# Performance work log

Hardware: AMD Instinct MI355X
Metric: run time of the kernel (lower is better)

## Reference

```python
import jax, jax.numpy as jnp
import numpy as np

B, T, D, H = 4, 2048, 1024, 16
HD = D // H  # head_dim = 64


def setup_inputs() -> dict:
    key = jax.random.key(0)
    k1, k2, k3 = jax.random.split(key, 3)
    x = jax.random.normal(k1, (B, T, D), dtype=jnp.float32)
    # Linear weights stored [in, out] (transpose of torch's [out, in]); scaled init.
    w_qkv = jax.random.normal(k2, (D, 3 * D), dtype=jnp.float32) / np.sqrt(D)
    b_qkv = jnp.zeros((3 * D,), dtype=jnp.float32)
    w_out = jax.random.normal(k3, (D, D), dtype=jnp.float32) / np.sqrt(D)
    b_out = jnp.zeros((D,), dtype=jnp.float32)
    # Causal mask [1,1,T,T]: 1 where attention allowed (j<=i), 0 elsewhere.
    causal_mask = jnp.tril(jnp.ones((T, T), dtype=jnp.int32))[None, None]
    return {"x": x, "causal_mask": causal_mask, "w_qkv": w_qkv,
            "b_qkv": b_qkv, "w_out": w_out, "b_out": b_out}


def reference(x, causal_mask, w_qkv, b_qkv, w_out, b_out):
    b, t, c = x.shape
    qkv = x @ w_qkv + b_qkv                         # [B,T,3D]
    qkv = qkv.reshape(b, t, 3, H, HD)
    q, k, v = jnp.moveaxis(qkv, 2, 0)               # each [B,T,H,HD]
    q = q.transpose(0, 2, 1, 3)                     # [B,H,T,HD]
    k = k.transpose(0, 2, 1, 3)
    v = v.transpose(0, 2, 1, 3)
    att = jnp.einsum('bhqd,bhkd->bhqk', q, k) / np.sqrt(HD).astype(np.float32)
    att = jnp.where(causal_mask == 0, jnp.float32(-jnp.inf), att)
    att = jax.nn.softmax(att, axis=-1)              # dropout=0.0 (eval)
    y = jnp.einsum('bhqk,bhkd->bhqd', att, v)       # [B,H,T,HD]
    y = y.transpose(0, 2, 1, 3).reshape(b, t, c)    # [B,T,D]
    return y @ w_out + b_out
```

## Files before the change

kernel.cpp:

```cpp
#include <hip/hip_runtime.h>
#include <hip/hip_bf16.h>
#include <stdint.h>

#define BB 4
#define TT 2048
#define DD 1024
#define HH 16
#define HDD 64
#define M1 (BB*TT)
#define N1 (3*DD)
#define KDIM DD

typedef __attribute__((ext_vector_type(8))) short short8;
typedef __attribute__((ext_vector_type(4))) float f32x4;

#if __has_builtin(__builtin_amdgcn_exp2f)
#define EXP2(x) __builtin_amdgcn_exp2f(x)
#else
#define EXP2(x) exp2f(x)
#endif

#define GLOAD_LDS16(gp, lp) \
    __builtin_amdgcn_global_load_lds( \
        (const __attribute__((address_space(1))) void*)(gp), \
        (__attribute__((address_space(3))) void*)(lp), 16, 0, 0)

__device__ __forceinline__ float bf2f(unsigned short u) {
    union { uint32_t u32; float f; } c; c.u32 = ((uint32_t)u) << 16; return c.f;
}
__device__ __forceinline__ unsigned short f2bf(float f) {
    union { float f; uint32_t u32; } c; c.f = f;
    uint32_t u = c.u32;
    return (unsigned short)((u + 0x7FFFu + ((u >> 16) & 1u)) >> 16);
}

template <int CTRL>
__device__ __forceinline__ float dpp_ror(float x) {
    union { float f; int i; } u, r;
    u.f = x;
    r.i = __builtin_amdgcn_update_dpp(u.i, u.i, CTRL, 0xF, 0xF, false);
    return r.f;
}
__device__ __forceinline__ float red_max16(float x) {
    x = fmaxf(x, dpp_ror<0x128>(x));
    x = fmaxf(x, dpp_ror<0x124>(x));
    x = fmaxf(x, dpp_ror<0x122>(x));
    x = fmaxf(x, dpp_ror<0x121>(x));
    return x;
}
__device__ __forceinline__ float red_sum16(float x) {
    x += dpp_ror<0x128>(x);
    x += dpp_ror<0x124>(x);
    x += dpp_ror<0x122>(x);
    x += dpp_ror<0x121>(x);
    return x;
}

__global__ __launch_bounds__(256) void cvt_f32_bf16(
    const float* __restrict__ in, unsigned short* __restrict__ out, int n4)
{
    int i = blockIdx.x * 256 + threadIdx.x;
    if (i >= n4) return;
    float4 v = *(const float4*)&in[(size_t)i * 4];
    ushort4 o;
    o.x = f2bf(v.x); o.y = f2bf(v.y); o.z = f2bf(v.z); o.w = f2bf(v.w);
    *(ushort4*)&out[(size_t)i * 4] = o;
}

__global__ __launch_bounds__(256) void transpose_f32_bf16(
    const float* __restrict__ in, unsigned short* __restrict__ out,
    int R, int C)
{
    __shared__ unsigned short tile[32][33];
    int bx = blockIdx.x;
    int by = blockIdx.y;
    int x = bx*32 + threadIdx.x;
    int y0 = by*32 + threadIdx.y;
    #pragma unroll
    for (int i = 0; i < 32; i += 8)
        tile[threadIdx.y + i][threadIdx.x] = f2bf(in[(size_t)(y0 + i)*C + x]);
    __syncthreads();
    int xo = by*32 + threadIdx.x;
    int yo = bx*32 + threadIdx.y;
    #pragma unroll
    for (int i = 0; i < 32; i += 8)
        out[(size_t)(yo + i)*R + xo] = tile[threadIdx.x][threadIdx.y + i];
}

#define GTSTR 264
template <int MODE>
__global__ __launch_bounds__(512, 2) void gemm8p(
    const unsigned short* __restrict__ A, const unsigned short* __restrict__ BT,
    const float* __restrict__ bias, void* __restrict__ Cout, void* __restrict__ Cout2,
    int K, int N, int NXT)
{
    constexpr int SHSZ = (MODE == 2) ? 256*GTSTR : 65536;
    __shared__ __align__(16) unsigned short Sh[SHSZ];

    const int tid  = threadIdx.x;
    const int lane = tid & 63;
    const int wave = tid >> 6;
    const int wm = wave >> 2, wn = wave & 3;
    const int quad = lane >> 4, l16 = lane & 15;

    const int nwg = gridDim.x, cpx = nwg >> 3;
    const int wg = (blockIdx.x & 7)*cpx + (blockIdx.x >> 3);
    const int by = wg / NXT, bx = wg - by*NXT;
    const int m0 = by*256, n0 = bx*256;

    f32x4 acc[8][4] = {};
    const int nk = K >> 6;

    auto SA = [&](int d, int h) -> unsigned short* { return &Sh[(d*2 + h)*16384]; };
    auto SB = [&](int d, int h) -> unsigned short* { return &Sh[(d*2 + h)*16384 + 8192]; };

    auto STG_A = [&](int d, int h, int t) {
        const int k0 = t << 6;
        unsigned short* dst = SA(d, h);
        #pragma unroll
        for (int p = 0; p < 2; ++p) {
            int c = p*512 + tid;
            int rl = c >> 3, ch = (c & 7) ^ (rl & 7);
            GLOAD_LDS16(&A[(size_t)(m0 + h*128 + rl)*K + k0 + ch*8], &dst[c*8]);
        }
    };
    auto STG_B = [&](int d, int h, int t) {
        const int k0 = t << 6;
        unsigned short* dst = SB(d, h);
        #pragma unroll
        for (int p = 0; p < 2; ++p) {
            int c = p*512 + tid;
            int rl = c >> 3, ch = (c & 7) ^ (rl & 7);
            GLOAD_LDS16(&BT[(size_t)(n0 + h*128 + rl)*K + k0 + ch*8], &dst[c*8]);
        }
    };
    auto RA = [&](int d, int mf, int kk) -> short8 {
        int rl = mf*16 + l16;
        return *(const short8*)&SA(d, wm)[rl*64 + (((kk*4 + quad) ^ (rl & 7))*8)];
    };
    auto RB = [&](int d, int nf, int kk) -> short8 {
        int rl = (wn & 1)*64 + nf*16 + l16;
        return *(const short8*)&SB(d, wn >> 1)[rl*64 + (((kk*4 + quad) ^ (rl & 7))*8)];
    };

    STG_A(0, 0, 0); STG_A(0, 1, 0); STG_B(0, 0, 0); STG_B(0, 1, 0);
    STG_A(1, 0, 1);
    asm volatile("s_waitcnt vmcnt(2)" ::: "memory");
    __builtin_amdgcn_s_barrier();
    __builtin_amdgcn_sched_barrier(0);

    for (int i = 0; i < nk/2; ++i) {
        const int tb = 2*i + 1, tn0 = 2*i + 2, tn1 = 2*i + 3;
        const bool p2 = (tn0 < nk), p3 = (tn1 < nk);
        short8 a0[4][2], a1[4][2], b0[2][2], b1[2][2];

        #pragma unroll
        for (int mf = 0; mf < 4; ++mf) { a0[mf][0] = RA(0, mf, 0); a0[mf][1] = RA(0, mf, 1); }
        #pragma unroll
        for (int nf = 0; nf < 2; ++nf) { b0[nf][0] = RB(0, nf, 0); b0[nf][1] = RB(0, nf, 1); }
        STG_A(1, 1, tb);
        __builtin_amdgcn_s_barrier();
        __builtin_amdgcn_s_setprio(1);
        #pragma unroll
        for (int mf = 0; mf < 4; ++mf)
            #pragma unroll
            for (int nf = 0; nf < 2; ++nf)
                #pragma unroll
                for (int kk = 0; kk < 2; ++kk)
                    acc[mf][nf] = __builtin_amdgcn_mfma_f32_16x16x32_bf16(
                        a0[mf][kk], b0[nf][kk], acc[mf][nf], 0, 0, 0);
        __builtin_amdgcn_s_setprio(0);
        __builtin_amdgcn_s_barrier();

        #pragma unroll
        for (int nf = 0; nf < 2; ++nf) { b1[nf][0] = RB(0, 2+nf, 0); b1[nf][1] = RB(0, 2+nf, 1); }
        STG_B(1, 0, tb);
        __builtin_amdgcn_s_barrier();
        __builtin_amdgcn_s_setprio(1);
        #pragma unroll
        for (int mf = 0; mf < 4; ++mf)
            #pragma unroll
            for (int nf = 0; nf < 2; ++nf)
                #pragma unroll
                for (int kk = 0; kk < 2; ++kk)
                    acc[mf][2+nf] = __builtin_amdgcn_mfma_f32_16x16x32_bf16(
                        a0[mf][kk], b1[nf][kk], acc[mf][2+nf], 0, 0, 0);
        __builtin_amdgcn_s_setprio(0);
        __builtin_amdgcn_s_barrier();

        #pragma unroll
        for (int mf = 0; mf < 4; ++mf) { a1[mf][0] = RA(0, 4+mf, 0); a1[mf][1] = RA(0, 4+mf, 1); }
        STG_B(1, 1, tb);
        __builtin_amdgcn_s_barrier();
        __builtin_amdgcn_s_setprio(1);
        #pragma unroll
        for (int mf = 0; mf < 4; ++mf)
            #pragma unroll
            for (int nf = 0; nf < 2; ++nf)
                #pragma unroll
                for (int kk = 0; kk < 2; ++kk)
                    acc[4+mf][nf] = __builtin_amdgcn_mfma_f32_16x16x32_bf16(
                        a1[mf][kk], b0[nf][kk], acc[4+mf][nf], 0, 0, 0);
        __builtin_amdgcn_s_setprio(0);
        __builtin_amdgcn_s_barrier();

        if (p2) STG_A(0, 0, tn0);
        __builtin_amdgcn_s_barrier();
        __builtin_amdgcn_s_setprio(1);
        #pragma unroll
        for (int mf = 0; mf < 4; ++mf)
            #pragma unroll
            for (int nf = 0; nf < 2; ++nf)
                #pragma unroll
                for (int kk = 0; kk < 2; ++kk)
                    acc[4+mf][2+nf] = __builtin_amdgcn_mfma_f32_16x16x32_bf16(
                        a1[mf][kk], b1[nf][kk], acc[4+mf][2+nf], 0, 0, 0);
        __builtin_amdgcn_s_setprio(0);
        if (p2) asm volatile("s_waitcnt vmcnt(2)" ::: "memory");
        else    asm volatile("s_waitcnt vmcnt(0)" ::: "memory");
        __builtin_amdgcn_s_barrier();
        __builtin_amdgcn_sched_barrier(0);

        #pragma unroll
        for (int mf = 0; mf < 4; ++mf) { a0[mf][0] = RA(1, mf, 0); a0[mf][1] = RA(1, mf, 1); }
        #pragma unroll
        for (int nf = 0; nf < 2; ++nf) { b0[nf][0] = RB(1, nf, 0); b0[nf][1] = RB(1, nf, 1); }
        if (p2) STG_A(0, 1, tn0);
        __builtin_amdgcn_s_barrier();
        __builtin_amdgcn_s_setprio(1);
        #pragma unroll
        for (int mf = 0; mf < 4; ++mf)
            #pragma unroll
            for (int nf = 0; nf < 2; ++nf)
                #pragma unroll
                for (int kk = 0; kk < 2; ++kk)
                    acc[mf][nf] = __builtin_amdgcn_mfma_f32_16x16x32_bf16(
                        a0[mf][kk], b0[nf][kk], acc[mf][nf], 0, 0, 0);
        __builtin_amdgcn_s_setprio(0);
        __builtin_amdgcn_s_barrier();

        #pragma unroll
        for (int nf = 0; nf < 2; ++nf) { b1[nf][0] = RB(1, 2+nf, 0); b1[nf][1] = RB(1, 2+nf, 1); }
        if (p2) STG_B(0, 0, tn0);
        __builtin_amdgcn_s_barrier();
        __builtin_amdgcn_s_setprio(1);
        #pragma unroll
        for (int mf = 0; mf < 4; ++mf)
            #pragma unroll
            for (int nf = 0; nf < 2; ++nf)
                #pragma unroll
                for (int kk = 0; kk < 2; ++kk)
                    acc[mf][2+nf] = __builtin_amdgcn_mfma_f32_16x16x32_bf16(
                        a0[mf][kk], b1[nf][kk], acc[mf][2+nf], 0, 0, 0);
        __builtin_amdgcn_s_setprio(0);
        __builtin_amdgcn_s_barrier();

        #pragma unroll
        for (int mf = 0; mf < 4; ++mf) { a1[mf][0] = RA(1, 4+mf, 0); a1[mf][1] = RA(1, 4+mf, 1); }
        if (p2) STG_B(0, 1, tn0);
        __builtin_amdgcn_s_barrier();
        __builtin_amdgcn_s_setprio(1);
        #pragma unroll
        for (int mf = 0; mf < 4; ++mf)
            #pragma unroll
            for (int nf = 0; nf < 2; ++nf)
                #pragma unroll
                for (int kk = 0; kk < 2; ++kk)
                    acc[4+mf][nf] = __builtin_amdgcn_mfma_f32_16x16x32_bf16(
                        a1[mf][kk], b0[nf][kk], acc[4+mf][nf], 0, 0, 0);
        __builtin_amdgcn_s_setprio(0);
        __builtin_amdgcn_s_barrier();

        if (p3) STG_A(1, 0, tn1);
        __builtin_amdgcn_s_barrier();
        __builtin_amdgcn_s_setprio(1);
        #pragma unroll
        for (int mf = 0; mf < 4; ++mf)
            #pragma unroll
            for (int nf = 0; nf < 2; ++nf)
                #pragma unroll
                for (int kk = 0; kk < 2; ++kk)
                    acc[4+mf][2+nf] = __builtin_amdgcn_mfma_f32_16x16x32_bf16(
                        a1[mf][kk], b1[nf][kk], acc[4+mf][2+nf], 0, 0, 0);
        __builtin_amdgcn_s_setprio(0);
        if (p3) asm volatile("s_waitcnt vmcnt(2)" ::: "memory");
        else    asm volatile("s_waitcnt vmcnt(0)" ::: "memory");
        __builtin_amdgcn_s_barrier();
        __builtin_amdgcn_sched_barrier(0);
    }

    if (MODE == 2 && n0 >= 2048) {
        #pragma unroll
        for (int ni = 0; ni < 4; ++ni) {
            int nl = wn*64 + ni*16 + l16;
            float bv = bias[n0 + nl];
            #pragma unroll
            for (int mi = 0; mi < 8; ++mi) {
                ushort4 pk;
                pk.x = f2bf(acc[mi][ni][0] + bv);
                pk.y = f2bf(acc[mi][ni][1] + bv);
                pk.z = f2bf(acc[mi][ni][2] + bv);
                pk.w = f2bf(acc[mi][ni][3] + bv);
                *(ushort4*)&Sh[nl*GTSTR + wm*128 + mi*16 + quad*4] = pk;
            }
        }
        __builtin_amdgcn_s_barrier();
        const int bb = m0 >> 11, t0 = m0 & 2047;
        #pragma unroll
        for (int p = 0; p < 16; ++p) {
            int c = p*512 + tid;
            int row = c >> 5, ch = c & 31;
            int nv = n0 + row - 2048;
            int hv = nv >> 6, dv = nv & 63;
            *(uint4*)&((unsigned short*)Cout2)[((size_t)((bb*16 + hv)*64 + dv))*2048 + t0 + ch*8] =
                *(uint4*)&Sh[row*GTSTR + ch*8];
        }
        return;
    }

    const int cstride = (MODE == 2) ? 2048 : N;
    #pragma unroll
    for (int ni = 0; ni < 4; ++ni) {
        int n = n0 + wn*64 + ni*16 + l16;
        float bv = bias[n];
        #pragma unroll
        for (int mi = 0; mi < 8; ++mi) {
            #pragma unroll
            for (int r = 0; r < 4; ++r) {
                int m = m0 + wm*128 + mi*16 + quad*4 + r;
                float val = acc[mi][ni][r] + bv;
                if (MODE == 1)
                    ((float*)Cout)[(size_t)m*cstride + n] = val;
                else
                    ((unsigned short*)Cout)[(size_t)m*cstride + n] = f2bf(val);
            }
        }
    }
}

template <int MODE, int BM, int BN>
__global__ __launch_bounds__(512, 2) void gemm_big(
    const unsigned short* __restrict__ A, const unsigned short* __restrict__ BT,
    const float* __restrict__ bias, void* __restrict__ Cout, void* __restrict__ Cout2,
    int K, int N, int NXT)
{
    constexpr int SHSZ = 2*(BM+BN)*64;
    __shared__ __align__(16) unsigned short Sh[SHSZ];

    const int tid  = threadIdx.x;
    const int lane = tid & 63;
    const int wave = tid >> 6;
    constexpr int WNG = BN/64;
    const int wm = wave / WNG, wn = wave % WNG;
    const int quad = lane >> 4, l16 = lane & 15;

    const int nwg = gridDim.x, cpx = nwg >> 3;
    const int wg = (blockIdx.x & 7)*cpx + (blockIdx.x >> 3);
    const int by = wg / NXT, bx = wg - by*NXT;
    const int m0 = by*BM, n0 = bx*BN;

    f32x4 acc[4][4] = {};
    const int nk = K >> 6;

    auto STAGE = [&](int t, int buf) {
        const int k0 = t << 6;
        unsigned short* Ab = &Sh[buf*(BM*64)];
        unsigned short* Bb = &Sh[2*BM*64 + buf*(BN*64)];
        #pragma unroll
        for (int p = 0; p < BM/64; ++p) {
            int c = p*512 + tid;
            int row = c >> 3, ch = (c & 7) ^ (row & 7);
            GLOAD_LDS16(&A[(size_t)(m0 + row)*K + k0 + ch*8], &Ab[c*8]);
        }
        #pragma unroll
        for (int p = 0; p < BN/64; ++p) {
            int c = p*512 + tid;
            int row = c >> 3, ch = (c & 7) ^ (row & 7);
            GLOAD_LDS16(&BT[(size_t)(n0 + row)*K + k0 + ch*8], &Bb[c*8]);
        }
    };

    STAGE(0, 0);
    STAGE(1, 1);

    for (int t = 0; t < nk; ++t) {
        const int buf = t & 1;
        const unsigned short* Ab = &Sh[buf*(BM*64)];
        const unsigned short* Bb = &Sh[2*BM*64 + buf*(BN*64)];

        if (t == nk - 1) asm volatile("s_waitcnt vmcnt(0)" ::: "memory");
        else             asm volatile("s_waitcnt vmcnt(6)" ::: "memory");
        __builtin_amdgcn_s_barrier();
        __builtin_amdgcn_sched_barrier(0);

        short8 fa[4][2], fb[2][2];

        #pragma unroll
        for (int mi = 0; mi < 4; ++mi)
            #pragma unroll
            for (int kk = 0; kk < 2; ++kk) {
                int row = wm*64 + mi*16 + l16;
                fa[mi][kk] = *(const short8*)&Ab[row*64 + (((kk*4 + quad) ^ (row & 7))*8)];
            }
        #pragma unroll
        for (int ni = 0; ni < 2; ++ni)
            #pragma unroll
            for (int kk = 0; kk < 2; ++kk) {
                int row = wn*64 + ni*16 + l16;
                fb[ni][kk] = *(const short8*)&Bb[row*64 + (((kk*4 + quad) ^ (row & 7))*8)];
            }
        __builtin_amdgcn_s_barrier();
        __builtin_amdgcn_s_setprio(1);
        #pragma unroll
        for (int mi = 0; mi < 4; ++mi)
            #pragma unroll
            for (int ni = 0; ni < 2; ++ni)
                #pragma unroll
                for (int kk = 0; kk < 2; ++kk)
                    acc[mi][ni] = __builtin_amdgcn_mfma_f32_16x16x32_bf16(
                        fa[mi][kk], fb[ni][kk], acc[mi][ni], 0, 0, 0);
        __builtin_amdgcn_s_setprio(0);
        __builtin_amdgcn_s_barrier();

        #pragma unroll
        for (int ni = 0; ni < 2; ++ni)
            #pragma unroll
            for (int kk = 0; kk < 2; ++kk) {
                int row = wn*64 + 32 + ni*16 + l16;
                fb[ni][kk] = *(const short8*)&Bb[row*64 + (((kk*4 + quad) ^ (row & 7))*8)];
            }
        __builtin_amdgcn_s_barrier();
        __builtin_amdgcn_s_setprio(1);
        #pragma unroll
        for (int mi = 0; mi < 4; ++mi)
            #pragma unroll
            for (int ni = 0; ni < 2; ++ni)
                #pragma unroll
                for (int kk = 0; kk < 2; ++kk)
                    acc[mi][2 + ni] = __builtin_amdgcn_mfma_f32_16x16x32_bf16(
                        fa[mi][kk], fb[ni][kk], acc[mi][2 + ni], 0, 0, 0);
        __builtin_amdgcn_s_setprio(0);
        __builtin_amdgcn_s_barrier();

        __builtin_amdgcn_sched_barrier(0);
        if (t + 2 < nk) STAGE(t + 2, buf);
    }

    const int cstride = (MODE == 2) ? 2048 : N;
    #pragma unroll
    for (int ni = 0; ni < 4; ++ni) {
        int n = n0 + wn*64 + ni*16 + l16;
        float bv = bias[n];
        #pragma unroll
        for (int mi = 0; mi < 4; ++mi) {
            #pragma unroll
            for (int r = 0; r < 4; ++r) {
                int m = m0 + wm*64 + mi*16 + quad*4 + r;
                float val = acc[mi][ni][r] + bv;
                if (MODE == 1)
                    ((float*)Cout)[(size_t)m*cstride + n] = val;
                else
                    ((unsigned short*)Cout)[(size_t)m*cstride + n] = f2bf(val);
            }
        }
    }
}

#define PST 72
__global__ __launch_bounds__(256, 3) void attn_mfma(
    const unsigned short* __restrict__ QK, const unsigned short* __restrict__ VT,
    unsigned short* __restrict__ Y)
{
    __shared__ __align__(16) unsigned short Sh[16384 + 4*32*PST];

    const int tid  = threadIdx.x;
    const int lane = tid & 63;
    const int wave = tid >> 6;
    const int quad = lane >> 4, l16 = lane & 15;

    const int i = blockIdx.x;
    const int xcd = i & 7, j = i >> 3;
    const int a = j & 7;
    const int u = j >> 3;
    const int bh2 = xcd + 8*u;
    const int b = bh2 >> 4, h = bh2 & 15;
    const size_t qkbase = (size_t)(b*TT) * 2048;
    const size_t vbase  = (size_t)(bh2*64) * 2048;
    const int qcol = h*64, kcol = 1024 + h*64;
    const float C2 = 0.18033688011112042f;

    unsigned short* Pw = &Sh[16384 + wave*(32*PST)];

    const int nk1 = 2*a + 2;
    const int ntot = 34;

    short8 aq[2][2];
    f32x4 o[2][4];
    float mold[2][4], lsum[2][4];
    int q0w = a*128 + wave*32;

    auto LOADQ = [&]() {
        #pragma unroll
        for (int mt = 0; mt < 2; ++mt)
            #pragma unroll
            for (int kk = 0; kk < 2; ++kk)
                aq[mt][kk] = *(const short8*)&QK[qkbase + (size_t)(q0w + mt*16 + l16)*2048
                                                + qcol + kk*32 + quad*8];
        #pragma unroll
        for (int mt = 0; mt < 2; ++mt)
            #pragma unroll
            for (int r = 0; r < 4; ++r) { mold[mt][r] = -3.0e38f; lsum[mt][r] = 0.0f; }
        #pragma unroll
        for (int mt = 0; mt < 2; ++mt)
            #pragma unroll
            for (int dt = 0; dt < 4; ++dt) { f32x4 z = {}; o[mt][dt] = z; }
    };
    auto FINALIZE = [&]() {
        #pragma unroll
        for (int mt = 0; mt < 2; ++mt)
            #pragma unroll
            for (int r = 0; r < 4; ++r) {
                float inv = 1.0f / lsum[mt][r];
                int tq = q0w + mt*16 + quad*4 + r;
                #pragma unroll
                for (int dt = 0; dt < 4; ++dt)
                    Y[((size_t)(b*TT + tq))*DD + h*64 + dt*16 + l16] = f2bf(o[mt][dt][r] * inv);
            }
    };

    auto STAGE = [&](int buf, int k0) {
        unsigned short* Kb = &Sh[buf*4096];
        unsigned short* Vb = &Sh[8192 + buf*4096];
        #pragma unroll
        for (int p = 0; p < 2; ++p) {
            int c = p*256 + tid;
            int r = c >> 3;
            int ch = (c & 7) ^ (r & 7);
            GLOAD_LDS16(&QK[qkbase + (size_t)(k0 + r)*2048 + kcol + ch*8], &Kb[c*8]);
        }
        #pragma unroll
        for (int p = 0; p < 2; ++p) {
            int c = p*256 + tid;
            int r = c >> 3;
            int ch = (c & 7) ^ (r & 7);
            GLOAD_LDS16(&VT[vbase + (size_t)r*2048 + k0 + ch*8], &Vb[c*8]);
        }
    };

    LOADQ();
    STAGE(0, 0);
    asm volatile("s_waitcnt vmcnt(0)" ::: "memory");
    __builtin_amdgcn_s_barrier();

    int cur = 0;
    for (int t = 0; t < ntot; ++t) {
        const int k0 = ((t < nk1) ? t : t - nk1) * 64;
        if (t + 1 < ntot) {
            const int t1 = t + 1;
            STAGE(cur ^ 1, ((t1 < nk1) ? t1 : t1 - nk1) * 64);
        }
        if (t == nk1) {
            FINALIZE();
            q0w = (15 - a)*128 + wave*32;
            LOADQ();
        }

        if (k0 <= q0w + 31) {
            const unsigned short* Kb = &Sh[cur*4096];
            const unsigned short* Vb = &Sh[8192 + cur*4096];

            f32x4 s[2][4];
            #pragma unroll
            for (int nt = 0; nt < 4; ++nt) {
                if (k0 + nt*16 <= q0w + 31) {
                    f32x4 z = {};
                    s[0][nt] = z; s[1][nt] = z;
                    #pragma unroll
                    for (int kk = 0; kk < 2; ++kk) {
                        int r = nt*16 + l16;
                        short8 bk = *(const short8*)&Kb[r*64 + (((kk*4 + quad) ^ (r & 7))*8)];
                        s[0][nt] = __builtin_amdgcn_mfma_f32_16x16x32_bf16(aq[0][kk], bk, s[0][nt], 0, 0, 0);
                        s[1][nt] = __builtin_amdgcn_mfma_f32_16x16x32_bf16(aq[1][kk], bk, s[1][nt], 0, 0, 0);
                    }
                } else {
                    #pragma unroll
                    for (int r = 0; r < 4; ++r) { s[0][nt][r] = -3.0e38f; s[1][nt][r] = -3.0e38f; }
                }
            }

            short8 bv[2][4];
            #pragma unroll
            for (int kk = 0; kk < 2; ++kk)
                #pragma unroll
                for (int dt = 0; dt < 4; ++dt) {
                    int r = dt*16 + l16;
                    bv[kk][dt] = *(const short8*)&Vb[r*64 + (((kk*4 + quad) ^ (r & 7))*8)];
                }

            if (k0 + 63 > q0w) {
                #pragma unroll
                for (int mt = 0; mt < 2; ++mt)
                    #pragma unroll
                    for (int nt = 0; nt < 4; ++nt)
                        #pragma unroll
                        for (int r = 0; r < 4; ++r) {
                            int kg = k0 + nt*16 + l16;
                            int qg = q0w + mt*16 + quad*4 + r;
                            if (kg > qg) s[mt][nt][r] = -3.0e38f;
                        }
            }

            float m2n[2][4], al[2][4];
            #pragma unroll
            for (int mt = 0; mt < 2; ++mt)
                #pragma unroll
                for (int r = 0; r < 4; ++r) {
                    float rm = fmaxf(fmaxf(s[mt][0][r], s[mt][1][r]),
                                     fmaxf(s[mt][2][r], s[mt][3][r]));
                    rm = red_max16(rm);
                    float m2 = fmaxf(mold[mt][r], rm * C2);
                    al[mt][r]  = EXP2(mold[mt][r] - m2);
                    m2n[mt][r] = m2;
                }
            float rs[2][4] = {};
            #pragma unroll
            for (int mt = 0; mt < 2; ++mt)
                #pragma unroll
                for (int nt = 0; nt < 4; ++nt)
                    #pragma unroll
                    for (int r = 0; r < 4; ++r) {
                        float p = EXP2(fmaf(s[mt][nt][r], C2, -m2n[mt][r]));
                        s[mt][nt][r] = p;
                        rs[mt][r] += p;
                    }
            #pragma unroll
            for (int mt = 0; mt < 2; ++mt)
                #pragma unroll
                for (int r = 0; r < 4; ++r) {
                    float tsum = red_sum16(rs[mt][r]);
                    lsum[mt][r] = lsum[mt][r]*al[mt][r] + tsum;
                    mold[mt][r] = m2n[mt][r];
                }

            #pragma unroll
            for (int mt = 0; mt < 2; ++mt)
                #pragma unroll
                for (int nt = 0; nt < 4; ++nt)
                    #pragma unroll
                    for (int r = 0; r < 4; ++r) {
                        union { float f; uint32_t u; } c; c.f = s[mt][nt][r];
                        Pw[(mt*16 + quad*4 + r)*PST + nt*16 + l16] =
                            (unsigned short)((c.u + 0x8000u) >> 16);
                    }

            #pragma unroll
            for (int mt = 0; mt < 2; ++mt)
                #pragma unroll
                for (int dt = 0; dt < 4; ++dt)
                    #pragma unroll
                    for (int r = 0; r < 4; ++r)
                        o[mt][dt][r] *= al[mt][r];
            #pragma unroll
            for (int kk = 0; kk < 2; ++kk) {
                short8 ap0 = *(short8*)&Pw[(     l16)*PST + kk*32 + quad*8];
                short8 ap1 = *(short8*)&Pw[(16 + l16)*PST + kk*32 + quad*8];
                #pragma unroll
                for (int dt = 0; dt < 4; ++dt) {
                    o[0][dt] = __builtin_amdgcn_mfma_f32_16x16x32_bf16(ap0, bv[kk][dt], o[0][dt], 0, 0, 0);
                    o[1][dt] = __builtin_amdgcn_mfma_f32_16x16x32_bf16(ap1, bv[kk][dt], o[1][dt], 0, 0, 0);
                }
            }
        }

        asm volatile("s_waitcnt vmcnt(0)" ::: "memory");
        __builtin_amdgcn_s_barrier();
        cur ^= 1;
    }

    FINALIZE();
}

extern "C" void kernel_launch(void* const* d_in, const int* in_sizes, int n_in,
                              void* d_out, int out_size, void* d_ws, size_t ws_size,
                              hipStream_t stream)
{
    const float* x    = (const float*)d_in[0];
    const float* wqkv = (const float*)d_in[2];
    const float* bqkv = (const float*)d_in[3];
    const float* wout = (const float*)d_in[4];
    const float* bout = (const float*)d_in[5];
    float* out = (float*)d_out;

    char* ws = (char*)d_ws;
    unsigned short* Xb    = (unsigned short*)ws;
    unsigned short* WqkvT = (unsigned short*)(ws + 16777216);
    unsigned short* WoutT = (unsigned short*)(ws + 23068672);
    unsigned short* QK    = (unsigned short*)(ws + 25165824);
    unsigned short* VTb   = (unsigned short*)(ws + 58720256);
    unsigned short* Ybuf  = (unsigned short*)(ws + 75497472);

    cvt_f32_bf16<<<(M1*KDIM/4 + 255)/256, 256, 0, stream>>>(x, Xb, M1*KDIM/4);
    transpose_f32_bf16<<<dim3(N1/32, KDIM/32), dim3(32, 8), 0, stream>>>(wqkv, WqkvT, KDIM, N1);
    transpose_f32_bf16<<<dim3(DD/32, KDIM/32), dim3(32, 8), 0, stream>>>(wout, WoutT, KDIM, DD);
    gemm8p<2><<<dim3(384), 512, 0, stream>>>(Xb, WqkvT, bqkv, QK, VTb, KDIM, N1, 12);
    attn_mfma<<<dim3(512), 256, 0, stream>>>(QK, VTb, Ybuf);
    gemm_big<1, 128, 256><<<dim3(256), 512, 0, stream>>>(Ybuf, WoutT, bout, out, nullptr, KDIM, DD, 4);
}
```

Measured before the change: 312.3 us.

## Split paired causal query chunks into separate blocks, heaviest-first order

```diff
diff --git a/kernel.cpp b/kernel.cpp
--- a/kernel.cpp
+++ b/kernel.cpp
@@ -480,8 +480,8 @@
 
     const int i = blockIdx.x;
     const int xcd = i & 7, j = i >> 3;
-    const int a = j & 7;
-    const int u = j >> 3;
+    const int qc = 15 - (j >> 3);
+    const int u = j & 7;
     const int bh2 = xcd + 8*u;
     const int b = bh2 >> 4, h = bh2 & 15;
     const size_t qkbase = (size_t)(b*TT) * 2048;
@@ -491,42 +491,23 @@
 
     unsigned short* Pw = &Sh[16384 + wave*(32*PST)];
 
-    const int nk1 = 2*a + 2;
-    const int ntot = 34;
+    const int nkt = 2*qc + 2;
+    const int q0w = qc*128 + wave*32;
 
     short8 aq[2][2];
-    f32x4 o[2][4];
+    #pragma unroll
+    for (int mt = 0; mt < 2; ++mt)
+        #pragma unroll
+        for (int kk = 0; kk < 2; ++kk)
+            aq[mt][kk] = *(const short8*)&QK[qkbase + (size_t)(q0w + mt*16 + l16)*2048
+                                            + qcol + kk*32 + quad*8];
+
+    f32x4 o[2][4] = {};
     float mold[2][4], lsum[2][4];
-    int q0w = a*128 + wave*32;
-
-    auto LOADQ = [&]() {
-        #pragma unroll
-        for (int mt = 0; mt < 2; ++mt)
-            #pragma unroll
-            for (int kk = 0; kk < 2; ++kk)
-                aq[mt][kk] = *(const short8*)&QK[qkbase + (size_t)(q0w + mt*16 + l16)*2048
-                                                + qcol + kk*32 + quad*8];
-        #pragma unroll
-        for (int mt = 0; mt < 2; ++mt)
-            #pragma unroll
-            for (int r = 0; r < 4; ++r) { mold[mt][r] = -3.0e38f; lsum[mt][r] = 0.0f; }
-        #pragma unroll
-        for (int mt = 0; mt < 2; ++mt)
-            #pragma unroll
-            for (int dt = 0; dt < 4; ++dt) { f32x4 z = {}; o[mt][dt] = z; }
-    };
-    auto FINALIZE = [&]() {
-        #pragma unroll
-        for (int mt = 0; mt < 2; ++mt)
-            #pragma unroll
-            for (int r = 0; r < 4; ++r) {
-                float inv = 1.0f / lsum[mt][r];
-                int tq = q0w + mt*16 + quad*4 + r;
-                #pragma unroll
-                for (int dt = 0; dt < 4; ++dt)
-                    Y[((size_t)(b*TT + tq))*DD + h*64 + dt*16 + l16] = f2bf(o[mt][dt][r] * inv);
-            }
-    };
+    #pragma unroll
+    for (int mt = 0; mt < 2; ++mt)
+        #pragma unroll
+        for (int r = 0; r < 4; ++r) { mold[mt][r] = -3.0e38f; lsum[mt][r] = 0.0f; }
 
     auto STAGE = [&](int buf, int k0) {
         unsigned short* Kb = &Sh[buf*4096];
@@ -547,23 +528,14 @@
         }
     };
 
-    LOADQ();
     STAGE(0, 0);
     asm volatile("s_waitcnt vmcnt(0)" ::: "memory");
     __builtin_amdgcn_s_barrier();
 
     int cur = 0;
-    for (int t = 0; t < ntot; ++t) {
-        const int k0 = ((t < nk1) ? t : t - nk1) * 64;
-        if (t + 1 < ntot) {
-            const int t1 = t + 1;
-            STAGE(cur ^ 1, ((t1 < nk1) ? t1 : t1 - nk1) * 64);
-        }
-        if (t == nk1) {
-            FINALIZE();
-            q0w = (15 - a)*128 + wave*32;
-            LOADQ();
-        }
+    for (int t = 0; t < nkt; ++t) {
+        const int k0 = t * 64;
+        if (t + 1 < nkt) STAGE(cur ^ 1, (t + 1) * 64);
 
         if (k0 <= q0w + 31) {
             const unsigned short* Kb = &Sh[cur*4096];
@@ -677,7 +649,16 @@
         cur ^= 1;
     }
 
-    FINALIZE();
+    #pragma unroll
+    for (int mt = 0; mt < 2; ++mt)
+        #pragma unroll
+        for (int r = 0; r < 4; ++r) {
+            float inv = 1.0f / lsum[mt][r];
+            int tq = q0w + mt*16 + quad*4 + r;
+            #pragma unroll
+            for (int dt = 0; dt < 4; ++dt)
+                Y[((size_t)(b*TT + tq))*DD + h*64 + dt*16 + l16] = f2bf(o[mt][dt][r] * inv);
+        }
 }
 
 extern "C" void kernel_launch(void* const* d_in, const int* in_sizes, int n_in,
@@ -703,6 +684,6 @@
     transpose_f32_bf16<<<dim3(N1/32, KDIM/32), dim3(32, 8), 0, stream>>>(wqkv, WqkvT, KDIM, N1);
     transpose_f32_bf16<<<dim3(DD/32, KDIM/32), dim3(32, 8), 0, stream>>>(wout, WoutT, KDIM, DD);
     gemm8p<2><<<dim3(384), 512, 0, stream>>>(Xb, WqkvT, bqkv, QK, VTb, KDIM, N1, 12);
-    attn_mfma<<<dim3(512), 256, 0, stream>>>(QK, VTb, Ybuf);
+    attn_mfma<<<dim3(1024), 256, 0, stream>>>(QK, VTb, Ybuf);
     gemm_big<1, 128, 256><<<dim3(256), 512, 0, stream>>>(Ybuf, WoutT, bout, out, nullptr, KDIM, DD, 4);
 }
```

After: 292.5 us. 6.3% less time.
